# Performance work log

Measured on AMD Instinct MI355X. Metric: run time of the kernel, lower is better.

The kernel has to match this reference:

```python
import jax, jax.numpy as jnp
import numpy as np

B, S, W, D, T = 64, 512, 384, 768, 21


def setup_inputs() -> dict:
    key = jax.random.key(0)
    ks = jax.random.split(key, 8)
    hidden_states = jax.random.normal(ks[0], (B, S, D), dtype=jnp.float32)  # BERT last_hidden_state
    word_maps = jnp.sort(jax.random.randint(ks[1], (B, W), 0, S), axis=1)  # first-subword index per word
    tags = jax.random.randint(ks[2], (B, W), 0, T)
    word_mask = jnp.ones((B, W), dtype=bool)  # torchcrf requires mask[:,0] all on
    W_tag = jax.random.normal(ks[3], (T, D), dtype=jnp.float32) * 0.02  # hidden2tag weight
    b_tag = jnp.zeros((T,), dtype=jnp.float32)
    start_trans = jax.random.uniform(ks[4], (T,), minval=-0.1, maxval=0.1)
    end_trans = jax.random.uniform(ks[5], (T,), minval=-0.1, maxval=0.1)
    trans = jax.random.uniform(ks[6], (T, T), minval=-0.1, maxval=0.1)
    return dict(hidden_states=hidden_states, W_tag=W_tag, b_tag=b_tag,
                start_trans=start_trans, end_trans=end_trans, trans=trans,
                word_maps=word_maps, tags=tags, word_mask=word_mask)


def reference(hidden_states, W_tag, b_tag, start_trans, end_trans, trans,
              word_maps, tags, word_mask):
    # --- ragged subword -> word gather (vectorized form of the python loop) ---
    word_feats = jnp.take_along_axis(hidden_states, word_maps[:, :, None], axis=1)  # [B,W,D]
    # dropout is identity in eval / deterministic reference
    emissions = jnp.einsum('bwd,td->bwt', word_feats, W_tag) + b_tag  # [B,W,T]

    maskf = word_mask.astype(emissions.dtype)
    bidx = jnp.arange(tags.shape[0])

    # --- CRF numerator: score of the given tag sequence ---
    emit_sc = jnp.take_along_axis(emissions, tags[:, :, None], axis=2)[..., 0]  # [B,W]
    trans_sc = trans[tags[:, :-1], tags[:, 1:]]                                  # [B,W-1]
    num = start_trans[tags[:, 0]] + emit_sc[:, 0]
    num = num + jnp.sum((trans_sc + emit_sc[:, 1:]) * maskf[:, 1:], axis=1)
    lengths = word_mask.sum(axis=1)
    last_tags = jnp.take_along_axis(tags, (lengths - 1)[:, None], axis=1)[:, 0]
    num = num + end_trans[last_tags]

    # --- CRF denominator: log partition via forward recurrence (scan over time) ---
    def step(score, xm):
        em_t, m_t = xm  # [B,T], [B]
        nxt = jax.nn.logsumexp(score[:, :, None] + trans[None, :, :] + em_t[:, None, :], axis=1)
        return jnp.where(m_t[:, None], nxt, score), None

    score0 = start_trans[None, :] + emissions[:, 0]  # [B,T]
    score, _ = jax.lax.scan(step, score0,
                            (jnp.swapaxes(emissions[:, 1:], 0, 1), word_mask[:, 1:].T))
    log_z = jax.nn.logsumexp(score + end_trans[None, :], axis=1)  # [B]

    llh = num - log_z
    return -jnp.mean(llh)  # reduction='mean', negated
```

## Files before the change

### kernel.cpp

```cpp
#include <hip/hip_runtime.h>
#include <math.h>

#define BB 64
#define SS 512
#define WW 384
#define DD 768
#define TT 21
#define ROWS (BB*WW)
#define EMSTRIDE (WW*TT)
#define NCH 16
#define CLEN 24
#define PSTRIDE 24
#define PMATSZ (TT*PSTRIDE)
#define PTSZ (PSTRIDE*PSTRIDE)
#define LN32 3.4657359027997265f

typedef short   bf16x8 __attribute__((ext_vector_type(8)));
typedef float   f32x4  __attribute__((ext_vector_type(4)));
union FragU { bf16x8 v; unsigned u[4]; };

__device__ __forceinline__ unsigned pack_bf16(unsigned lo, unsigned hi) {
    return __builtin_amdgcn_perm(hi, lo, 0x07060302);
}

__global__ __launch_bounds__(256) void emissions_kernel(
    const float* __restrict__ hidden, const int* __restrict__ word_maps,
    const float* __restrict__ W_tag, const float* __restrict__ b_tag,
    float* __restrict__ em, float* __restrict__ out)
{
    __shared__ __align__(16) unsigned short Bs[24 * 2 * 4 * 16 * 8];
    __shared__ __align__(16) float Sred[2][64][8];
    __shared__ int rowoff[32];

    const int tid = threadIdx.x;
    const int rowBase = blockIdx.x * 32;

    if (blockIdx.x == 0 && tid == 0) out[0] = 0.0f;

    if (tid < 32) {
        int row = rowBase + tid;
        int b = row / WW;
        int w = row - b * WW;
        rowoff[tid] = b * SS + word_maps[b * WW + w];
    }

    for (int i = tid; i < TT * (DD / 4); i += 256) {
        int t = i / (DD / 4), q = i - t * (DD / 4);
        int k  = q * 4;
        int ks = k >> 5, quad = (k >> 3) & 3, e = k & 7;
        int nt = t >> 4, l16 = t & 15;
        float4 wv = *(const float4*)&W_tag[t * DD + k];
        int off = ((ks * 2 + nt) * 4 + quad) * 128 + l16 * 8 + e;
        *(unsigned*)&Bs[off]     = pack_bf16(__float_as_uint(wv.x), __float_as_uint(wv.y));
        *(unsigned*)&Bs[off + 2] = pack_bf16(__float_as_uint(wv.z), __float_as_uint(wv.w));
    }
    __syncthreads();

    const int wv_  = tid >> 6;
    const int rt   = wv_ >> 1;
    const int h    = wv_ & 1;
    const int lane = tid & 63;
    const int l16  = lane & 15;
    const int quad = lane >> 4;

    const float* abase = hidden + (size_t)rowoff[rt * 16 + l16] * DD
                                + h * (DD / 2) + quad * 8;
    const unsigned short* bbase = Bs + quad * 128 + l16 * 8 + h * 12 * 1024;

    f32x4 acc0 = {}, acc1 = {};

    float4 A0[4], A1[4];
    #pragma unroll
    for (int p = 0; p < 4; ++p) {
        A0[p] = *(const float4*)(abase + p * 32);
        A1[p] = *(const float4*)(abase + p * 32 + 4);
    }
    bf16x8 b0c = *(const bf16x8*)(bbase);
    bf16x8 b1c = *(const bf16x8*)(bbase + 512);

    #pragma unroll
    for (int ks = 0; ks < 12; ++ks) {
        bf16x8 b0n = b0c, b1n = b1c;
        if (ks < 11) {
            b0n = *(const bf16x8*)(bbase + (ks + 1) * 1024);
            b1n = *(const bf16x8*)(bbase + (ks + 1) * 1024 + 512);
        }
        FragU a;
        a.u[0] = pack_bf16(__float_as_uint(A0[ks & 3].x), __float_as_uint(A0[ks & 3].y));
        a.u[1] = pack_bf16(__float_as_uint(A0[ks & 3].z), __float_as_uint(A0[ks & 3].w));
        a.u[2] = pack_bf16(__float_as_uint(A1[ks & 3].x), __float_as_uint(A1[ks & 3].y));
        a.u[3] = pack_bf16(__float_as_uint(A1[ks & 3].z), __float_as_uint(A1[ks & 3].w));
        if (ks < 8) {
            A0[ks & 3] = *(const float4*)(abase + (ks + 4) * 32);
            A1[ks & 3] = *(const float4*)(abase + (ks + 4) * 32 + 4);
        }
        acc0 = __builtin_amdgcn_mfma_f32_16x16x32_bf16(a.v, b0c, acc0, 0, 0, 0);
        acc1 = __builtin_amdgcn_mfma_f32_16x16x32_bf16(a.v, b1c, acc1, 0, 0, 0);
        b0c = b0n; b1c = b1n;
    }

    if (h == 1) {
        #pragma unroll
        for (int r = 0; r < 4; ++r) {
            Sred[rt][lane][r]     = acc0[r];
            Sred[rt][lane][r + 4] = acc1[r];
        }
    }
    __syncthreads();

    if (h == 0) {
        #pragma unroll
        for (int r = 0; r < 4; ++r) {
            acc0[r] += Sred[rt][lane][r];
            acc1[r] += Sred[rt][lane][r + 4];
        }
        int rbase = rowBase + rt * 16 + quad * 4;
        {
            float bt = b_tag[l16];
            #pragma unroll
            for (int r = 0; r < 4; ++r)
                em[(size_t)(rbase + r) * TT + l16] = acc0[r] + bt;
        }
        if (16 + l16 < TT) {
            float bt = b_tag[16 + l16];
            #pragma unroll
            for (int r = 0; r < 4; ++r)
                em[(size_t)(rbase + r) * TT + 16 + l16] = acc1[r] + bt;
        }
    }
}

__global__ __launch_bounds__(256, 1) void chunk_kernel(
    const float* __restrict__ em, const float* __restrict__ trans,
    float* __restrict__ Pmat)
{
    __shared__ __align__(16) float Es[PTSZ];
    __shared__ __align__(16) float Pbuf[4][2][PMATSZ];
    __shared__ __align__(16) float gem[4][CLEN * PSTRIDE];

    const int tid  = threadIdx.x;
    const int wid  = tid >> 6;
    const int lane = tid & 63;
    const int id   = blockIdx.x * 4 + wid;
    const int b    = id >> 4;
    const int c    = id & (NCH - 1);
    const int s0   = 1 + c * CLEN;
    const int n    = (c == NCH - 1) ? (WW - s0) : CLEN;

    for (int idx = tid; idx < PTSZ; idx += 256) {
        int k = idx / PSTRIDE, j = idx - k * PSTRIDE;
        Es[idx] = (k < TT && j < TT) ? __expf(trans[k * TT + j]) * 0.03125f : 0.f;
    }

    int i3r = lane / 6;
    const int jg  = lane - i3r * 6;
    const bool active = (i3r < 7) && (jg < 6);
    const int i3 = (i3r < 7) ? i3r : 6;
    const int jbase = (jg < 6 ? jg : 5) * 4;

    for (int idx = lane; idx < n * PSTRIDE; idx += 64) {
        int tt = idx / PSTRIDE, j = idx - tt * PSTRIDE;
        float g = 1.0f;
        if (j < TT) g = __expf(em[((size_t)b * WW + (s0 + tt)) * TT + j]);
        gem[wid][idx] = g;
    }
    __syncthreads();

    {
        float4 g = *(const float4*)&gem[wid][jbase];
        #pragma unroll
        for (int r = 0; r < 3; ++r) {
            int i = i3 * 3 + r;
            float4 e = *(const float4*)&Es[i * PSTRIDE + jbase];
            float4 v = make_float4(e.x * g.x, e.y * g.y, e.z * g.z, e.w * g.w);
            if (active) *(float4*)&Pbuf[wid][0][i * PSTRIDE + jbase] = v;
        }
    }

    int pp = 0;
    for (int tt = 1; tt < n; ++tt) {
        float acc[3][4];
        #pragma unroll
        for (int r = 0; r < 3; ++r)
            #pragma unroll
            for (int q = 0; q < 4; ++q) acc[r][q] = 0.f;

        const float* Pc = &Pbuf[wid][pp][0];
        #pragma unroll
        for (int kb = 0; kb < 6; ++kb) {
            float4 p0 = *(const float4*)&Pc[(i3 * 3 + 0) * PSTRIDE + kb * 4];
            float4 p1 = *(const float4*)&Pc[(i3 * 3 + 1) * PSTRIDE + kb * 4];
            float4 p2 = *(const float4*)&Pc[(i3 * 3 + 2) * PSTRIDE + kb * 4];
            #pragma unroll
            for (int kk = 0; kk < 4; ++kk) {
                const int k = kb * 4 + kk;
                float4 e = *(const float4*)&Es[k * PSTRIDE + jbase];
                float a = (kk == 0) ? p0.x : (kk == 1) ? p0.y : (kk == 2) ? p0.z : p0.w;
                float bv= (kk == 0) ? p1.x : (kk == 1) ? p1.y : (kk == 2) ? p1.z : p1.w;
                float cv= (kk == 0) ? p2.x : (kk == 1) ? p2.y : (kk == 2) ? p2.z : p2.w;
                acc[0][0] = fmaf(a, e.x, acc[0][0]); acc[0][1] = fmaf(a, e.y, acc[0][1]);
                acc[0][2] = fmaf(a, e.z, acc[0][2]); acc[0][3] = fmaf(a, e.w, acc[0][3]);
                acc[1][0] = fmaf(bv, e.x, acc[1][0]); acc[1][1] = fmaf(bv, e.y, acc[1][1]);
                acc[1][2] = fmaf(bv, e.z, acc[1][2]); acc[1][3] = fmaf(bv, e.w, acc[1][3]);
                acc[2][0] = fmaf(cv, e.x, acc[2][0]); acc[2][1] = fmaf(cv, e.y, acc[2][1]);
                acc[2][2] = fmaf(cv, e.z, acc[2][2]); acc[2][3] = fmaf(cv, e.w, acc[2][3]);
            }
        }
        float4 g = *(const float4*)&gem[wid][tt * PSTRIDE + jbase];
        if (active) {
            #pragma unroll
            for (int r = 0; r < 3; ++r) {
                float4 v = make_float4(acc[r][0] * g.x, acc[r][1] * g.y,
                                       acc[r][2] * g.z, acc[r][3] * g.w);
                *(float4*)&Pbuf[wid][1 - pp][(i3 * 3 + r) * PSTRIDE + jbase] = v;
            }
        }
        pp ^= 1;
    }

    float* dst = Pmat + (size_t)id * PTSZ;
    const float* Pf = &Pbuf[wid][pp][0];
    for (int idx = lane; idx < PTSZ; idx += 64) {
        int j = idx / PSTRIDE, i = idx - j * PSTRIDE;
        dst[idx] = (i < TT) ? Pf[i * PSTRIDE + j] : 0.f;
    }
}

__device__ __forceinline__ float lane_bcast(float v, int l) {
    return __uint_as_float(__builtin_amdgcn_readlane(__float_as_uint(v), l));
}

__global__ __launch_bounds__(64, 1) void combine_kernel(
    const float* __restrict__ Pmat, const float* __restrict__ em,
    const int* __restrict__ tags, const float* __restrict__ start_trans,
    const float* __restrict__ end_trans, const float* __restrict__ trans,
    float* __restrict__ out)
{
    const int b = blockIdx.x;
    const int j = threadIdx.x;
    const bool act = (j < TT);
    const int jc = act ? j : (TT - 1);
    const float* emb = em + (size_t)b * EMSTRIDE;

    float s0v = start_trans[jc] + emb[jc];
    float M = act ? s0v : -1e30f;
    #pragma unroll
    for (int o = 32; o > 0; o >>= 1) M = fmaxf(M, __shfl_xor(M, o));
    float sig = act ? __expf(s0v - M) : 0.0f;

    for (int c = 0; c < NCH; ++c) {
        const float* PT = Pmat + (size_t)(b * NCH + c) * PTSZ + jc * PSTRIDE;
        float4 c0 = *(const float4*)&PT[0];
        float4 c1 = *(const float4*)&PT[4];
        float4 c2 = *(const float4*)&PT[8];
        float4 c3 = *(const float4*)&PT[12];
        float4 c4 = *(const float4*)&PT[16];
        float  c5 = PT[20];
        float col[TT];
        col[0]=c0.x;  col[1]=c0.y;  col[2]=c0.z;  col[3]=c0.w;
        col[4]=c1.x;  col[5]=c1.y;  col[6]=c1.z;  col[7]=c1.w;
        col[8]=c2.x;  col[9]=c2.y;  col[10]=c2.z; col[11]=c2.w;
        col[12]=c3.x; col[13]=c3.y; col[14]=c3.z; col[15]=c3.w;
        col[16]=c4.x; col[17]=c4.y; col[18]=c4.z; col[19]=c4.w;
        col[20]=c5;
        float a0 = 0.f, a1 = 0.f, a2 = 0.f;
        #pragma unroll
        for (int i = 0; i < TT; i += 3) {
            a0 = fmaf(lane_bcast(sig, i    ), col[i    ], a0);
            a1 = fmaf(lane_bcast(sig, i + 1), col[i + 1], a1);
            a2 = fmaf(lane_bcast(sig, i + 2), col[i + 2], a2);
        }
        float v = act ? (a0 + a1 + a2) : 0.0f;
        float m = v;
        #pragma unroll
        for (int o = 32; o > 0; o >>= 1) m = fmaxf(m, __shfl_xor(m, o));
        int nst = (c == NCH - 1) ? (WW - (1 + c * CLEN)) : CLEN;
        M += __logf(m) + (float)nst * LN32;
        sig = v / m;
    }

    float fin = (act && sig > 0.f) ? (M + __logf(sig) + end_trans[jc]) : -1e30f;
    float mm = fin;
    #pragma unroll
    for (int o = 32; o > 0; o >>= 1) mm = fmaxf(mm, __shfl_xor(mm, o));
    float pe = __expf(fin - mm);
    float ssum = pe;
    #pragma unroll
    for (int o = 32; o > 0; o >>= 1) ssum += __shfl_xor(ssum, o);
    float lz = mm + __logf(ssum);

    const int* tb = tags + b * WW;
    float part = 0.f;
    for (int w = j; w < WW; w += 64) {
        int tw = tb[w];
        float e = emb[w * TT + tw];
        float tsc = (w == 0) ? start_trans[tw] : trans[tb[w - 1] * TT + tw];
        part += tsc + e;
    }
    #pragma unroll
    for (int o = 32; o > 0; o >>= 1) part += __shfl_xor(part, o);

    if (j == 0) {
        float num = part + end_trans[tb[WW - 1]];
        atomicAdd(out, -(num - lz) * (1.0f / BB));
    }
}

extern "C" void kernel_launch(void* const* d_in, const int* in_sizes, int n_in,
                              void* d_out, int out_size, void* d_ws, size_t ws_size,
                              hipStream_t stream) {
    const float* hidden      = (const float*)d_in[0];
    const float* W_tag       = (const float*)d_in[1];
    const float* b_tag       = (const float*)d_in[2];
    const float* start_trans = (const float*)d_in[3];
    const float* end_trans   = (const float*)d_in[4];
    const float* trans       = (const float*)d_in[5];
    const int*   word_maps   = (const int*)  d_in[6];
    const int*   tags        = (const int*)  d_in[7];

    float* out  = (float*)d_out;
    float* em   = (float*)d_ws;
    float* Pmat = (float*)d_ws + (size_t)ROWS * TT;

    emissions_kernel<<<ROWS / 32, 256, 0, stream>>>(hidden, word_maps, W_tag, b_tag, em, out);
    chunk_kernel<<<BB * NCH / 4, 256, 0, stream>>>(em, trans, Pmat);
    combine_kernel<<<BB, 64, 0, stream>>>(Pmat, em, tags, start_trans, end_trans, trans, out);
}
```

Measured before the change: 195.3 us.

## Restructure CRF chunk kernel: row-per-lane chains, more shorter chunks, prefetch in combine

Splits the sequence into 24 chunks of 16 instead of 16 of 24, which shortens the serial matrix-product chain per chunk and raises the number of independent chunks. Each 64-thread block now handles three chunks, with each lane owning one full row of the running product in registers. This removes the per-step shared-memory ping-pong between lanes. The combine kernel software-prefetches the next chunk's transfer column while computing the current one. The trade-offs are a longer sequential combine loop (24 steps), higher register pressure, and idle lanes (one of 64 per block).

Result: slower. 457.4 us (+134.2%).

```diff
diff --git a/kernel.cpp b/kernel.cpp
--- a/kernel.cpp
+++ b/kernel.cpp
@@ -8,10 +8,9 @@
 #define TT 21
 #define ROWS (BB*WW)
 #define EMSTRIDE (WW*TT)
-#define NCH 16
-#define CLEN 24
+#define NCH 24
+#define CLEN 16
 #define PSTRIDE 24
-#define PMATSZ (TT*PSTRIDE)
 #define PTSZ (PSTRIDE*PSTRIDE)
 #define LN32 3.4657359027997265f
 
@@ -130,99 +129,91 @@
     }
 }
 
-__global__ __launch_bounds__(256, 1) void chunk_kernel(
+__global__ __launch_bounds__(64, 2) void chunk_kernel(
     const float* __restrict__ em, const float* __restrict__ trans,
     float* __restrict__ Pmat)
 {
     __shared__ __align__(16) float Es[PTSZ];
-    __shared__ __align__(16) float Pbuf[4][2][PMATSZ];
-    __shared__ __align__(16) float gem[4][CLEN * PSTRIDE];
-
-    const int tid  = threadIdx.x;
-    const int wid  = tid >> 6;
-    const int lane = tid & 63;
-    const int id   = blockIdx.x * 4 + wid;
-    const int b    = id >> 4;
-    const int c    = id & (NCH - 1);
-    const int s0   = 1 + c * CLEN;
-    const int n    = (c == NCH - 1) ? (WW - s0) : CLEN;
-
-    for (int idx = tid; idx < PTSZ; idx += 256) {
+    __shared__ __align__(16) float gem[3][CLEN][PSTRIDE];
+    __shared__ __align__(16) float Ptmp[3][PSTRIDE][PSTRIDE];
+
+    const int lane  = threadIdx.x;
+    const int qbase = blockIdx.x * 3;
+
+    for (int idx = lane; idx < PTSZ; idx += 64) {
         int k = idx / PSTRIDE, j = idx - k * PSTRIDE;
         Es[idx] = (k < TT && j < TT) ? __expf(trans[k * TT + j]) * 0.03125f : 0.f;
     }
-
-    int i3r = lane / 6;
-    const int jg  = lane - i3r * 6;
-    const bool active = (i3r < 7) && (jg < 6);
-    const int i3 = (i3r < 7) ? i3r : 6;
-    const int jbase = (jg < 6 ? jg : 5) * 4;
-
-    for (int idx = lane; idx < n * PSTRIDE; idx += 64) {
-        int tt = idx / PSTRIDE, j = idx - tt * PSTRIDE;
+    for (int idx = lane; idx < 3 * CLEN * PSTRIDE; idx += 64) {
+        int cc  = idx / (CLEN * PSTRIDE);
+        int rem = idx - cc * (CLEN * PSTRIDE);
+        int tt  = rem / PSTRIDE, j = rem - tt * PSTRIDE;
+        int q = qbase + cc;
+        int bq = q / NCH, c = q - bq * NCH;
+        int word = 1 + c * CLEN + tt;
         float g = 1.0f;
-        if (j < TT) g = __expf(em[((size_t)b * WW + (s0 + tt)) * TT + j]);
-        gem[wid][idx] = g;
+        if (j < TT && word < WW) g = __expf(em[((size_t)bq * WW + word) * TT + j]);
+        gem[cc][tt][j] = g;
     }
     __syncthreads();
 
-    {
-        float4 g = *(const float4*)&gem[wid][jbase];
-        #pragma unroll
-        for (int r = 0; r < 3; ++r) {
-            int i = i3 * 3 + r;
-            float4 e = *(const float4*)&Es[i * PSTRIDE + jbase];
-            float4 v = make_float4(e.x * g.x, e.y * g.y, e.z * g.z, e.w * g.w);
-            if (active) *(float4*)&Pbuf[wid][0][i * PSTRIDE + jbase] = v;
-        }
-    }
-
-    int pp = 0;
+    int sub = lane / 21;
+    int row = lane - sub * 21;
+    const bool act = (sub < 3);
+    if (!act) { sub = 2; row = 20; }
+
+    const int q  = qbase + sub;
+    const int c  = q - (q / NCH) * NCH;
+    const int n  = (c == NCH - 1) ? (WW - (1 + c * CLEN)) : CLEN;
+
+    float rw[PSTRIDE];
+    float ac[PSTRIDE];
+
+    #pragma unroll
+    for (int jb = 0; jb < 6; ++jb) {
+        float4 e = *(const float4*)&Es[row * PSTRIDE + jb * 4];
+        float4 g = *(const float4*)&gem[sub][0][jb * 4];
+        rw[jb*4+0] = e.x * g.x; rw[jb*4+1] = e.y * g.y;
+        rw[jb*4+2] = e.z * g.z; rw[jb*4+3] = e.w * g.w;
+    }
+
     for (int tt = 1; tt < n; ++tt) {
-        float acc[3][4];
-        #pragma unroll
-        for (int r = 0; r < 3; ++r)
+        #pragma unroll
+        for (int j = 0; j < PSTRIDE; ++j) ac[j] = 0.f;
+        #pragma unroll
+        for (int k = 0; k < PSTRIDE; ++k) {
+            float rk = rw[k];
             #pragma unroll
-            for (int q = 0; q < 4; ++q) acc[r][q] = 0.f;
-
-        const float* Pc = &Pbuf[wid][pp][0];
-        #pragma unroll
-        for (int kb = 0; kb < 6; ++kb) {
-            float4 p0 = *(const float4*)&Pc[(i3 * 3 + 0) * PSTRIDE + kb * 4];
-            float4 p1 = *(const float4*)&Pc[(i3 * 3 + 1) * PSTRIDE + kb * 4];
-            float4 p2 = *(const float4*)&Pc[(i3 * 3 + 2) * PSTRIDE + kb * 4];
-            #pragma unroll
-            for (int kk = 0; kk < 4; ++kk) {
-                const int k = kb * 4 + kk;
-                float4 e = *(const float4*)&Es[k * PSTRIDE + jbase];
-                float a = (kk == 0) ? p0.x : (kk == 1) ? p0.y : (kk == 2) ? p0.z : p0.w;
-                float bv= (kk == 0) ? p1.x : (kk == 1) ? p1.y : (kk == 2) ? p1.z : p1.w;
-                float cv= (kk == 0) ? p2.x : (kk == 1) ? p2.y : (kk == 2) ? p2.z : p2.w;
-                acc[0][0] = fmaf(a, e.x, acc[0][0]); acc[0][1] = fmaf(a, e.y, acc[0][1]);
-                acc[0][2] = fmaf(a, e.z, acc[0][2]); acc[0][3] = fmaf(a, e.w, acc[0][3]);
-                acc[1][0] = fmaf(bv, e.x, acc[1][0]); acc[1][1] = fmaf(bv, e.y, acc[1][1]);
-                acc[1][2] = fmaf(bv, e.z, acc[1][2]); acc[1][3] = fmaf(bv, e.w, acc[1][3]);
-                acc[2][0] = fmaf(cv, e.x, acc[2][0]); acc[2][1] = fmaf(cv, e.y, acc[2][1]);
-                acc[2][2] = fmaf(cv, e.z, acc[2][2]); acc[2][3] = fmaf(cv, e.w, acc[2][3]);
+            for (int jb = 0; jb < 6; ++jb) {
+                float4 e = *(const float4*)&Es[k * PSTRIDE + jb * 4];
+                ac[jb*4+0] = fmaf(rk, e.x, ac[jb*4+0]);
+                ac[jb*4+1] = fmaf(rk, e.y, ac[jb*4+1]);
+                ac[jb*4+2] = fmaf(rk, e.z, ac[jb*4+2]);
+                ac[jb*4+3] = fmaf(rk, e.w, ac[jb*4+3]);
             }
         }
-        float4 g = *(const float4*)&gem[wid][tt * PSTRIDE + jbase];
-        if (active) {
-            #pragma unroll
-            for (int r = 0; r < 3; ++r) {
-                float4 v = make_float4(acc[r][0] * g.x, acc[r][1] * g.y,
-                                       acc[r][2] * g.z, acc[r][3] * g.w);
-                *(float4*)&Pbuf[wid][1 - pp][(i3 * 3 + r) * PSTRIDE + jbase] = v;
-            }
-        }
-        pp ^= 1;
-    }
-
-    float* dst = Pmat + (size_t)id * PTSZ;
-    const float* Pf = &Pbuf[wid][pp][0];
-    for (int idx = lane; idx < PTSZ; idx += 64) {
-        int j = idx / PSTRIDE, i = idx - j * PSTRIDE;
-        dst[idx] = (i < TT) ? Pf[i * PSTRIDE + j] : 0.f;
+        #pragma unroll
+        for (int jb = 0; jb < 6; ++jb) {
+            float4 g = *(const float4*)&gem[sub][tt][jb * 4];
+            rw[jb*4+0] = ac[jb*4+0] * g.x; rw[jb*4+1] = ac[jb*4+1] * g.y;
+            rw[jb*4+2] = ac[jb*4+2] * g.z; rw[jb*4+3] = ac[jb*4+3] * g.w;
+        }
+    }
+
+    if (act) {
+        #pragma unroll
+        for (int jb = 0; jb < 6; ++jb) {
+            float4 v = make_float4(rw[jb*4+0], rw[jb*4+1], rw[jb*4+2], rw[jb*4+3]);
+            *(float4*)&Ptmp[sub][row][jb * 4] = v;
+        }
+    }
+    __syncthreads();
+
+    for (int idx = lane; idx < 3 * PTSZ; idx += 64) {
+        int cc  = idx / PTSZ;
+        int rem = idx - cc * PTSZ;
+        int j = rem / PSTRIDE, i = rem - j * PSTRIDE;
+        Pmat[(size_t)(qbase + cc) * PTSZ + rem] = (i < TT) ? Ptmp[cc][i][j] : 0.f;
     }
 }
 
@@ -248,35 +239,47 @@
     for (int o = 32; o > 0; o >>= 1) M = fmaxf(M, __shfl_xor(M, o));
     float sig = act ? __expf(s0v - M) : 0.0f;
 
+    const float* Pb = Pmat + (size_t)b * NCH * PTSZ + jc * PSTRIDE;
+    float4 a0 = *(const float4*)&Pb[0];
+    float4 a1 = *(const float4*)&Pb[4];
+    float4 a2 = *(const float4*)&Pb[8];
+    float4 a3 = *(const float4*)&Pb[12];
+    float4 a4 = *(const float4*)&Pb[16];
+    float  a5 = Pb[20];
+
     for (int c = 0; c < NCH; ++c) {
-        const float* PT = Pmat + (size_t)(b * NCH + c) * PTSZ + jc * PSTRIDE;
-        float4 c0 = *(const float4*)&PT[0];
-        float4 c1 = *(const float4*)&PT[4];
-        float4 c2 = *(const float4*)&PT[8];
-        float4 c3 = *(const float4*)&PT[12];
-        float4 c4 = *(const float4*)&PT[16];
-        float  c5 = PT[20];
+        int cn = (c + 1 < NCH) ? c + 1 : c;
+        const float* Pn = Pb + (size_t)cn * PTSZ;
+        float4 n0 = *(const float4*)&Pn[0];
+        float4 n1 = *(const float4*)&Pn[4];
+        float4 n2 = *(const float4*)&Pn[8];
+        float4 n3 = *(const float4*)&Pn[12];
+        float4 n4 = *(const float4*)&Pn[16];
+        float  n5 = Pn[20];
+
         float col[TT];
-        col[0]=c0.x;  col[1]=c0.y;  col[2]=c0.z;  col[3]=c0.w;
-        col[4]=c1.x;  col[5]=c1.y;  col[6]=c1.z;  col[7]=c1.w;
-        col[8]=c2.x;  col[9]=c2.y;  col[10]=c2.z; col[11]=c2.w;
-        col[12]=c3.x; col[13]=c3.y; col[14]=c3.z; col[15]=c3.w;
-        col[16]=c4.x; col[17]=c4.y; col[18]=c4.z; col[19]=c4.w;
-        col[20]=c5;
-        float a0 = 0.f, a1 = 0.f, a2 = 0.f;
+        col[0]=a0.x;  col[1]=a0.y;  col[2]=a0.z;  col[3]=a0.w;
+        col[4]=a1.x;  col[5]=a1.y;  col[6]=a1.z;  col[7]=a1.w;
+        col[8]=a2.x;  col[9]=a2.y;  col[10]=a2.z; col[11]=a2.w;
+        col[12]=a3.x; col[13]=a3.y; col[14]=a3.z; col[15]=a3.w;
+        col[16]=a4.x; col[17]=a4.y; col[18]=a4.z; col[19]=a4.w;
+        col[20]=a5;
+        float p0 = 0.f, p1 = 0.f, p2 = 0.f;
         #pragma unroll
         for (int i = 0; i < TT; i += 3) {
-            a0 = fmaf(lane_bcast(sig, i    ), col[i    ], a0);
-            a1 = fmaf(lane_bcast(sig, i + 1), col[i + 1], a1);
-            a2 = fmaf(lane_bcast(sig, i + 2), col[i + 2], a2);
-        }
-        float v = act ? (a0 + a1 + a2) : 0.0f;
+            p0 = fmaf(lane_bcast(sig, i    ), col[i    ], p0);
+            p1 = fmaf(lane_bcast(sig, i + 1), col[i + 1], p1);
+            p2 = fmaf(lane_bcast(sig, i + 2), col[i + 2], p2);
+        }
+        float v = act ? (p0 + p1 + p2) : 0.0f;
         float m = v;
         #pragma unroll
         for (int o = 32; o > 0; o >>= 1) m = fmaxf(m, __shfl_xor(m, o));
         int nst = (c == NCH - 1) ? (WW - (1 + c * CLEN)) : CLEN;
         M += __logf(m) + (float)nst * LN32;
         sig = v / m;
+
+        a0 = n0; a1 = n1; a2 = n2; a3 = n3; a4 = n4; a5 = n5;
     }
 
     float fin = (act && sig > 0.f) ? (M + __logf(sig) + end_trans[jc]) : -1e30f;
@@ -323,6 +326,6 @@
     float* Pmat = (float*)d_ws + (size_t)ROWS * TT;
 
     emissions_kernel<<<ROWS / 32, 256, 0, stream>>>(hidden, word_maps, W_tag, b_tag, em, out);
-    chunk_kernel<<<BB * NCH / 4, 256, 0, stream>>>(em, trans, Pmat);
+    chunk_kernel<<<BB * NCH / 3, 64, 0, stream>>>(em, trans, Pmat);
     combine_kernel<<<BB, 64, 0, stream>>>(Pmat, em, tags, start_trans, end_trans, trans, out);
 }
```

## Double chunk count for CRF scan and prefetch next chunk matrix in combine

Applied to the files above, without the earlier changes.

Splits the CRF forward recurrence into 32 chunks of 12 steps instead of 16 chunks of 24. This shortens each chunk's serial matrix-product chain and doubles the number of waves doing chunk work. The combine kernel now loads the next chunk's transfer-matrix column before computing the current step, to hide global load latency. The cost is twice as many sequential combine steps and twice the Pmat memory traffic.

Measured after the change: 195.2 us. About the same (-0.0%).

```diff
diff --git a/kernel.cpp b/kernel.cpp
--- a/kernel.cpp
+++ b/kernel.cpp
@@ -8,8 +8,8 @@
 #define TT 21
 #define ROWS (BB*WW)
 #define EMSTRIDE (WW*TT)
-#define NCH 16
-#define CLEN 24
+#define NCH 32
+#define CLEN 12
 #define PSTRIDE 24
 #define PMATSZ (TT*PSTRIDE)
 #define PTSZ (PSTRIDE*PSTRIDE)
@@ -142,8 +142,8 @@
     const int wid  = tid >> 6;
     const int lane = tid & 63;
     const int id   = blockIdx.x * 4 + wid;
-    const int b    = id >> 4;
-    const int c    = id & (NCH - 1);
+    const int b    = id / NCH;
+    const int c    = id - b * NCH;
     const int s0   = 1 + c * CLEN;
     const int n    = (c == NCH - 1) ? (WW - s0) : CLEN;
 
@@ -248,35 +248,47 @@
     for (int o = 32; o > 0; o >>= 1) M = fmaxf(M, __shfl_xor(M, o));
     float sig = act ? __expf(s0v - M) : 0.0f;
 
+    const float* Pb = Pmat + (size_t)b * NCH * PTSZ + jc * PSTRIDE;
+    float4 a0 = *(const float4*)&Pb[0];
+    float4 a1 = *(const float4*)&Pb[4];
+    float4 a2 = *(const float4*)&Pb[8];
+    float4 a3 = *(const float4*)&Pb[12];
+    float4 a4 = *(const float4*)&Pb[16];
+    float  a5 = Pb[20];
+
     for (int c = 0; c < NCH; ++c) {
-        const float* PT = Pmat + (size_t)(b * NCH + c) * PTSZ + jc * PSTRIDE;
-        float4 c0 = *(const float4*)&PT[0];
-        float4 c1 = *(const float4*)&PT[4];
-        float4 c2 = *(const float4*)&PT[8];
-        float4 c3 = *(const float4*)&PT[12];
-        float4 c4 = *(const float4*)&PT[16];
-        float  c5 = PT[20];
+        int cn = (c + 1 < NCH) ? c + 1 : c;
+        const float* Pn = Pb + (size_t)cn * PTSZ;
+        float4 n0 = *(const float4*)&Pn[0];
+        float4 n1 = *(const float4*)&Pn[4];
+        float4 n2 = *(const float4*)&Pn[8];
+        float4 n3 = *(const float4*)&Pn[12];
+        float4 n4 = *(const float4*)&Pn[16];
+        float  n5 = Pn[20];
+
         float col[TT];
-        col[0]=c0.x;  col[1]=c0.y;  col[2]=c0.z;  col[3]=c0.w;
-        col[4]=c1.x;  col[5]=c1.y;  col[6]=c1.z;  col[7]=c1.w;
-        col[8]=c2.x;  col[9]=c2.y;  col[10]=c2.z; col[11]=c2.w;
-        col[12]=c3.x; col[13]=c3.y; col[14]=c3.z; col[15]=c3.w;
-        col[16]=c4.x; col[17]=c4.y; col[18]=c4.z; col[19]=c4.w;
-        col[20]=c5;
-        float a0 = 0.f, a1 = 0.f, a2 = 0.f;
+        col[0]=a0.x;  col[1]=a0.y;  col[2]=a0.z;  col[3]=a0.w;
+        col[4]=a1.x;  col[5]=a1.y;  col[6]=a1.z;  col[7]=a1.w;
+        col[8]=a2.x;  col[9]=a2.y;  col[10]=a2.z; col[11]=a2.w;
+        col[12]=a3.x; col[13]=a3.y; col[14]=a3.z; col[15]=a3.w;
+        col[16]=a4.x; col[17]=a4.y; col[18]=a4.z; col[19]=a4.w;
+        col[20]=a5;
+        float p0 = 0.f, p1 = 0.f, p2 = 0.f;
         #pragma unroll
         for (int i = 0; i < TT; i += 3) {
-            a0 = fmaf(lane_bcast(sig, i    ), col[i    ], a0);
-            a1 = fmaf(lane_bcast(sig, i + 1), col[i + 1], a1);
-            a2 = fmaf(lane_bcast(sig, i + 2), col[i + 2], a2);
-        }
-        float v = act ? (a0 + a1 + a2) : 0.0f;
+            p0 = fmaf(lane_bcast(sig, i    ), col[i    ], p0);
+            p1 = fmaf(lane_bcast(sig, i + 1), col[i + 1], p1);
+            p2 = fmaf(lane_bcast(sig, i + 2), col[i + 2], p2);
+        }
+        float v = act ? (p0 + p1 + p2) : 0.0f;
         float m = v;
         #pragma unroll
         for (int o = 32; o > 0; o >>= 1) m = fmaxf(m, __shfl_xor(m, o));
         int nst = (c == NCH - 1) ? (WW - (1 + c * CLEN)) : CLEN;
         M += __logf(m) + (float)nst * LN32;
         sig = v / m;
+
+        a0 = n0; a1 = n1; a2 = n2; a3 = n3; a4 = n4; a5 = n5;
     }
 
     float fin = (act && sig > 0.f) ? (M + __logf(sig) + end_trans[jc]) : -1e30f;
```
